# Kernel tuning notes

Measured on AMD Instinct MI355X. Metric: run time of the kernel, lower is better.

Reference implementation:

```python
import jax, jax.numpy as jnp
import numpy as np

GAMMA = 10.0  # params[('edge_penalty_gamma', 10.0, ...)]
EPS_SQRT = 1e-24  # guard for sqrt(0) (float_aware_sqrt)


def dXf(u, dx):
    # forward difference along axis -2, Neumann-zero boundary (replicate last row)
    return (jnp.concatenate([u[..., 1:, :], u[..., -1:, :]], axis=-2) - u) / dx


def dYf(u, dy):
    # forward difference along axis -1, Neumann-zero boundary (replicate last col)
    return (jnp.concatenate([u[..., :, 1:], u[..., :, -1:]], axis=-1) - u) / dy


def setup_inputs() -> dict:
    key = jax.random.key(0)
    k1, k2 = jax.random.split(key)
    B, K, H, W = 8, 8, 1024, 1024
    input_images = jax.random.normal(k1, (B, 1, H, W), dtype=jnp.float32)
    spacing = jnp.ones((2,), dtype=jnp.float32)
    label_probabilities = jax.random.uniform(k2, (B, K, H, W), dtype=jnp.float32)
    return {"input_images": input_images, "spacing": spacing,
            "label_probabilities": label_probabilities}


def reference(input_images, spacing, label_probabilities):
    # --- compute_localized_edge_penalty(I, spacing) ---
    I = input_images[:, 0, ...]                      # [B, H, W]
    sx, sy = spacing[0], spacing[1]
    gn2 = dXf(I, sx) ** 2 + dYf(I, sy) ** 2          # ||grad I||^2 (forward diffs)
    gnI = jnp.sqrt(jnp.maximum(gn2, EPS_SQRT))
    w_edge = 1.0 / (1.0 + GAMMA * gnI * jnp.min(spacing))  # [B, H, W]

    # --- normalized-cut relaxation over all clusters, fully batched ---
    p = label_probabilities                          # [B, K, H, W]
    # cut-cost stencil uses unit spacing (fd.FD_torch(spacing=[1.0]*dim))
    p_xp = dXf(p, 1.0)
    p_yp = dYf(p, 1.0)
    w = w_edge[:, None, :, :]                        # broadcast over clusters
    nom = jnp.sum(p * (p + w * (p_xp + p_yp)), axis=(-2, -1))   # [B, K]
    denom = jnp.sum(p * (1.0 + 2.0 * w), axis=(-2, -1))         # [B, K]
    cut_cost = nom / denom                                        # [B, K]

    B, K = p.shape[0], p.shape[1]
    current_penalties = K - jnp.sum(cut_cost, axis=1)            # [B]
    return jnp.sum(current_penalties)
```

## Files before the change

kernel.cpp:

```cpp
#include <hip/hip_runtime.h>


constexpr int Bsz  = 8;
constexpr int Kc   = 8;
constexpr int H    = 1024;
constexpr int W    = 1024;
constexpr int ROWS = 8;
constexpr int TPB  = 256;

#define GAMMA_F    10.0f
#define EPS_SQRT_F 1e-24f

__device__ __forceinline__ float wedge(float c, float dn, float rt,
                                       float inv_sx, float inv_sy, float smin) {
    float dx = (dn - c) * inv_sx;
    float dy = (rt - c) * inv_sy;
    float gn2 = dx * dx + dy * dy;
    float g = sqrtf(fmaxf(gn2, EPS_SQRT_F));
    return 1.0f / (1.0f + GAMMA_F * g * smin);
}

__device__ __forceinline__ void accum(float pc, float pd, float pr, float w,
                                      float& nom, float& den) {
    float lap = (pd - pc) + (pr - pc);
    nom = fmaf(pc, fmaf(w, lap, pc), nom);
    den = fmaf(pc, fmaf(2.0f, w, 1.0f), den);
}

__global__ __launch_bounds__(TPB) void cl_main(const float* __restrict__ I,
                                               const float* __restrict__ spacing,
                                               const float* __restrict__ P,
                                               double* __restrict__ ws) {
    const int t  = threadIdx.x;
    const int j0 = t * 4;
    const int b  = blockIdx.y;
    const int r0 = blockIdx.x * ROWS;

    const float sx = spacing[0], sy = spacing[1];
    const float inv_sx = 1.0f / sx, inv_sy = 1.0f / sy;
    const float smin = fminf(sx, sy);

    const int jr = (j0 + 4 < W) ? (j0 + 4) : (W - 1);

    const float* Ib = I + (size_t)b * H * W;
    const float* Pb = P + (size_t)b * Kc * H * W;

    float4 cI  = *(const float4*)(Ib + (size_t)r0 * W + j0);
    float  cIr = Ib[(size_t)r0 * W + jr];
    float4 cp[Kc];
    float  cpr[Kc];
#pragma unroll
    for (int k = 0; k < Kc; ++k) {
        const float* Pk = Pb + (size_t)k * H * W;
        cp[k]  = *(const float4*)(Pk + (size_t)r0 * W + j0);
        cpr[k] = Pk[(size_t)r0 * W + jr];
    }

    float nom[Kc], den[Kc];
#pragma unroll
    for (int k = 0; k < Kc; ++k) { nom[k] = 0.0f; den[k] = 0.0f; }

    for (int i = r0; i < r0 + ROWS; ++i) {
        const int inext = (i + 1 < H) ? (i + 1) : (H - 1);
        const float4 nI  = *(const float4*)(Ib + (size_t)inext * W + j0);
        const float  nIr = Ib[(size_t)inext * W + jr];

        const float w0 = wedge(cI.x, nI.x, cI.y, inv_sx, inv_sy, smin);
        const float w1 = wedge(cI.y, nI.y, cI.z, inv_sx, inv_sy, smin);
        const float w2 = wedge(cI.z, nI.z, cI.w, inv_sx, inv_sy, smin);
        const float w3 = wedge(cI.w, nI.w, cIr,  inv_sx, inv_sy, smin);

#pragma unroll
        for (int k = 0; k < Kc; ++k) {
            const float* Pk = Pb + (size_t)k * H * W;
            const float4 np  = *(const float4*)(Pk + (size_t)inext * W + j0);
            const float  npr = Pk[(size_t)inext * W + jr];

            accum(cp[k].x, np.x, cp[k].y, w0, nom[k], den[k]);
            accum(cp[k].y, np.y, cp[k].z, w1, nom[k], den[k]);
            accum(cp[k].z, np.z, cp[k].w, w2, nom[k], den[k]);
            accum(cp[k].w, np.w, cpr[k],  w3, nom[k], den[k]);

            cp[k]  = np;
            cpr[k] = npr;
        }
        cI  = nI;
        cIr = nIr;
    }

    __shared__ float red[4][2 * Kc];
    const int lane = t & 63;
    const int wave = t >> 6;

#pragma unroll
    for (int k = 0; k < Kc; ++k) {
        float n = nom[k], d = den[k];
#pragma unroll
        for (int off = 32; off > 0; off >>= 1) {
            n += __shfl_down(n, off, 64);
            d += __shfl_down(d, off, 64);
        }
        if (lane == 0) {
            red[wave][k]      = n;
            red[wave][Kc + k] = d;
        }
    }
    __syncthreads();

    if (t < 2 * Kc) {
        float s = red[0][t] + red[1][t] + red[2][t] + red[3][t];
        const int k = t & (Kc - 1);
        const int which = t >> 3;
        atomicAdd(&ws[(size_t)(b * Kc + k) * 2 + which], (double)s);
    }
}

__global__ void cl_final(const double* __restrict__ ws, float* __restrict__ out) {
    const int t = threadIdx.x;
    double c = 0.0;
    if (t < Bsz * Kc) {
        const double n = ws[(size_t)t * 2 + 0];
        const double d = ws[(size_t)t * 2 + 1];
        c = n / d;
    }
#pragma unroll
    for (int off = 32; off > 0; off >>= 1) c += __shfl_down(c, off, 64);
    if (t == 0) out[0] = (float)((double)(Bsz * Kc) - c);
}

extern "C" void kernel_launch(void* const* d_in, const int* in_sizes, int n_in,
                              void* d_out, int out_size, void* d_ws, size_t ws_size,
                              hipStream_t stream) {
    const float* I       = (const float*)d_in[0];
    const float* spacing = (const float*)d_in[1];
    const float* P       = (const float*)d_in[2];
    float* out = (float*)d_out;
    double* ws = (double*)d_ws;

    hipMemsetAsync(d_ws, 0, (size_t)Bsz * Kc * 2 * sizeof(double), stream);

    dim3 grid(H / ROWS, Bsz);
    cl_main<<<grid, TPB, 0, stream>>>(I, spacing, P, ws);
    cl_final<<<1, 64, 0, stream>>>(ws, out);
}
```

Baseline: 387.2 us.

## Replace double atomics with per-block partials and drop workspace memset

Each block now writes its per-cluster nom/den partial sums as float2 into a dedicated workspace slot instead of doing double-precision atomicAdd. The final kernel sums the 128 row-block partials per (b,k) in double. This removes the memset launch and the contention from atomics. The change also unrolls the row loop and adds an occupancy hint to launch_bounds. In exchange the final single-block kernel does a serial 128-step loop per thread, and the launch_bounds hint may constrain register allocation.

New measurement: 522.6 us. 1.35x slower.

```diff
diff --git a/kernel.cpp b/kernel.cpp
--- a/kernel.cpp
+++ b/kernel.cpp
@@ -6,6 +6,7 @@
 constexpr int H    = 1024;
 constexpr int W    = 1024;
 constexpr int ROWS = 8;
+constexpr int RB   = H / ROWS;
 constexpr int TPB  = 256;
 
 #define GAMMA_F    10.0f
@@ -27,10 +28,10 @@
     den = fmaf(pc, fmaf(2.0f, w, 1.0f), den);
 }
 
-__global__ __launch_bounds__(TPB) void cl_main(const float* __restrict__ I,
-                                               const float* __restrict__ spacing,
-                                               const float* __restrict__ P,
-                                               double* __restrict__ ws) {
+__global__ __launch_bounds__(TPB, 4) void cl_main(const float* __restrict__ I,
+                                                  const float* __restrict__ spacing,
+                                                  const float* __restrict__ P,
+                                                  float2* __restrict__ ws) {
     const int t  = threadIdx.x;
     const int j0 = t * 4;
     const int b  = blockIdx.y;
@@ -60,7 +61,9 @@
 #pragma unroll
     for (int k = 0; k < Kc; ++k) { nom[k] = 0.0f; den[k] = 0.0f; }
 
-    for (int i = r0; i < r0 + ROWS; ++i) {
+#pragma unroll
+    for (int ii = 0; ii < ROWS; ++ii) {
+        const int i = r0 + ii;
         const int inext = (i + 1 < H) ? (i + 1) : (H - 1);
         const float4 nI  = *(const float4*)(Ib + (size_t)inext * W + j0);
         const float  nIr = Ib[(size_t)inext * W + jr];
@@ -107,22 +110,24 @@
     }
     __syncthreads();
 
-    if (t < 2 * Kc) {
-        float s = red[0][t] + red[1][t] + red[2][t] + red[3][t];
-        const int k = t & (Kc - 1);
-        const int which = t >> 3;
-        atomicAdd(&ws[(size_t)(b * Kc + k) * 2 + which], (double)s);
+    if (t < Kc) {
+        const int k = t;
+        float n = red[0][k] + red[1][k] + red[2][k] + red[3][k];
+        float d = red[0][Kc + k] + red[1][Kc + k] + red[2][Kc + k] + red[3][Kc + k];
+        ws[((size_t)(b * RB + blockIdx.x)) * Kc + k] = make_float2(n, d);
     }
 }
 
-__global__ void cl_final(const double* __restrict__ ws, float* __restrict__ out) {
+__global__ void cl_final(const float2* __restrict__ ws, float* __restrict__ out) {
     const int t = threadIdx.x;
-    double c = 0.0;
-    if (t < Bsz * Kc) {
-        const double n = ws[(size_t)t * 2 + 0];
-        const double d = ws[(size_t)t * 2 + 1];
-        c = n / d;
+    const int b = t >> 3, k = t & 7;
+    double n = 0.0, d = 0.0;
+    for (int r = 0; r < RB; ++r) {
+        const float2 v = ws[((size_t)(b * RB + r)) * Kc + k];
+        n += (double)v.x;
+        d += (double)v.y;
     }
+    double c = n / d;
 #pragma unroll
     for (int off = 32; off > 0; off >>= 1) c += __shfl_down(c, off, 64);
     if (t == 0) out[0] = (float)((double)(Bsz * Kc) - c);
@@ -135,11 +140,9 @@
     const float* spacing = (const float*)d_in[1];
     const float* P       = (const float*)d_in[2];
     float* out = (float*)d_out;
-    double* ws = (double*)d_ws;
+    float2* ws = (float2*)d_ws;
 
-    hipMemsetAsync(d_ws, 0, (size_t)Bsz * Kc * 2 * sizeof(double), stream);
-
-    dim3 grid(H / ROWS, Bsz);
+    dim3 grid(RB, Bsz);
     cl_main<<<grid, TPB, 0, stream>>>(I, spacing, P, ws);
     cl_final<<<1, 64, 0, stream>>>(ws, out);
 }
```
